# Performance work log

Measured on AMD Instinct MI355X. Metric: run time of the kernel, lower is better.

Reference implementation:

```python
import jax, jax.numpy as jnp
import numpy as np

BN_EPS = 1e-5


def setup_inputs() -> dict:
    key = jax.random.key(0)
    ks = jax.random.split(key, 12)
    B, C, L, P = 8, 128, 4096, 96
    d = C // 8
    return {
        "x": jax.random.normal(ks[0], (B, C, 1), jnp.float32),
        "Wt": jax.random.normal(ks[1], (C, C, L), jnp.float32) * 0.02,
        "bt": jax.random.normal(ks[2], (C,), jnp.float32) * 0.02,
        "gamma": jnp.ones((C,), jnp.float32),
        "beta": jnp.zeros((C,), jnp.float32),
        "Wq": jax.random.normal(ks[3], (d, C), jnp.float32) * 0.05,
        "bq": jax.random.normal(ks[4], (d,), jnp.float32) * 0.02,
        "Wk": jax.random.normal(ks[5], (d, C), jnp.float32) * 0.05,
        "bk": jax.random.normal(ks[6], (d,), jnp.float32) * 0.02,
        "Wv": jax.random.normal(ks[7], (C, C), jnp.float32) * 0.05,
        "bv": jax.random.normal(ks[8], (C,), jnp.float32) * 0.02,
        "W2": jax.random.normal(ks[9], (P, C), jnp.float32) * 0.05,
        "b2": jax.random.normal(ks[10], (P,), jnp.float32) * 0.02,
    }


def reference(x, Wt, bt, gamma, beta, Wq, bq, Wk, bk, Wv, bv, W2, b2):
    # l1: ConvTranspose1d(C, C, kernel=L, stride=1) on input of length 1
    # out[b, o, l] = sum_i x[b, i, 0] * Wt[i, o, l] + bt[o]
    h = jnp.einsum('bi,iol->bol', x[:, :, 0], Wt) + bt[None, :, None]  # [B,C,L]
    # BatchNorm1d (training mode: batch stats, biased variance)
    mean = jnp.mean(h, axis=(0, 2), keepdims=True)
    var = jnp.mean((h - mean) ** 2, axis=(0, 2), keepdims=True)
    h = (h - mean) * jax.lax.rsqrt(var + BN_EPS)
    h = h * gamma[None, :, None] + beta[None, :, None]
    h = jax.nn.relu(h)
    # Self_Attn: 1x1 conv projections
    q = jnp.einsum('qc,bcl->bql', Wq, h) + bq[None, :, None]   # [B,d,L]
    k = jnp.einsum('qc,bcl->bql', Wk, h) + bk[None, :, None]   # [B,d,L]
    v = jnp.einsum('oc,bcl->bol', Wv, h) + bv[None, :, None]   # [B,C,L]
    energy = jnp.einsum('bdl,bdm->blm', q, k)                  # [B,L,L]
    attn = jax.nn.softmax(energy, axis=-1)
    out = jnp.einsum('bcm,blm->bcl', v, attn)                  # [B,C,L]
    # l2: Conv1d(C -> P, kernel=1)
    y = jnp.einsum('pc,bcl->bpl', W2, out) + b2[None, :, None]  # [B,P,L]
    return y
```

## Files before the change

### kernel.cpp

```cpp
#include <hip/hip_runtime.h>

#define B_ 8
#define C_ 128
#define L_ 4096
#define P_ 96
#define D_ 16

typedef __attribute__((ext_vector_type(8))) short short8;
typedef __attribute__((ext_vector_type(16))) float float16v;

__device__ __forceinline__ unsigned short f2bf(float f) {
  unsigned int u = __float_as_uint(f);
  u += 0x7fff + ((u >> 16) & 1);
  return (unsigned short)(u >> 16);
}

constexpr size_t OFF_H      = 0;
constexpr size_t OFF_PSUM   = 16777216;
constexpr size_t OFF_PSUMSQ = OFF_PSUM + 8192;
constexpr size_t OFF_SCALE  = OFF_PSUMSQ + 8192;
constexpr size_t OFF_SHIFT  = OFF_SCALE + 512;
constexpr size_t OFF_WALLT  = OFF_SHIFT + 512;
constexpr size_t OFF_BALL   = OFF_WALLT + 65536;
constexpr size_t OFF_QT     = OFF_BALL + 512;
constexpr size_t OFF_KT     = OFF_QT + 1048576;
constexpr size_t OFF_V2     = OFF_KT + 1048576;

__global__ __launch_bounds__(128) void k_prep(
    const float* __restrict__ Wq, const float* __restrict__ bq,
    const float* __restrict__ Wk, const float* __restrict__ bk,
    const float* __restrict__ Wv, const float* __restrict__ bv,
    const float* __restrict__ W2,
    float* __restrict__ wallT, float* __restrict__ ball)
{
  const int r = blockIdx.x;
  const int c = threadIdx.x;
  float wv;
  if (r < 16) {
    wv = Wq[r * C_ + c];
  } else if (r < 32) {
    wv = Wk[(r - 16) * C_ + c];
  } else {
    const int p = r - 32;
    float s = 0.f;
    for (int o = 0; o < C_; ++o) s += W2[p * C_ + o] * Wv[o * C_ + c];
    wv = s;
  }
  wallT[c * C_ + r] = wv;
  if (c == 0) {
    float bb;
    if (r < 16)      bb = bq[r];
    else if (r < 32) bb = bk[r - 16];
    else {
      const int p = r - 32;
      float s = 0.f;
      for (int o = 0; o < C_; ++o) s += W2[p * C_ + o] * bv[o];
      bb = s;
    }
    ball[r] = bb;
  }
}

__global__ __launch_bounds__(256) void k_conv(
    const float* __restrict__ x, const float* __restrict__ Wt,
    float* __restrict__ h, float* __restrict__ psum, float* __restrict__ psumsq)
{
  __shared__ float4 xs4[256];
  __shared__ float rs1[4], rs2[4];
  const int tid = threadIdx.x;
  const int o = blockIdx.y;
  const int l = blockIdx.x * 1024 + tid * 4;

  xs4[tid] = ((const float4*)x)[tid];
  __syncthreads();

  float4 acc[8];
#pragma unroll
  for (int bb = 0; bb < 8; ++bb) acc[bb] = (float4){0.f, 0.f, 0.f, 0.f};

  const float* wp = Wt + (size_t)o * L_ + l;
  const size_t stride = (size_t)C_ * L_;
#pragma unroll 2
  for (int i4 = 0; i4 < 32; ++i4) {
    const float4 w0 = *(const float4*)(wp + (size_t)(i4 * 4 + 0) * stride);
    const float4 w1 = *(const float4*)(wp + (size_t)(i4 * 4 + 1) * stride);
    const float4 w2 = *(const float4*)(wp + (size_t)(i4 * 4 + 2) * stride);
    const float4 w3 = *(const float4*)(wp + (size_t)(i4 * 4 + 3) * stride);
#pragma unroll
    for (int bb = 0; bb < 8; ++bb) {
      const float4 xb = xs4[bb * 32 + i4];
      acc[bb].x += xb.x * w0.x + xb.y * w1.x + xb.z * w2.x + xb.w * w3.x;
      acc[bb].y += xb.x * w0.y + xb.y * w1.y + xb.z * w2.y + xb.w * w3.y;
      acc[bb].z += xb.x * w0.z + xb.y * w1.z + xb.z * w2.z + xb.w * w3.z;
      acc[bb].w += xb.x * w0.w + xb.y * w1.w + xb.z * w2.w + xb.w * w3.w;
    }
  }
  float s1 = 0.f, s2 = 0.f;
#pragma unroll
  for (int bb = 0; bb < 8; ++bb) {
    *(float4*)(h + ((size_t)(bb * C_ + o)) * L_ + l) = acc[bb];
    s1 += acc[bb].x + acc[bb].y + acc[bb].z + acc[bb].w;
    s2 += acc[bb].x * acc[bb].x + acc[bb].y * acc[bb].y
        + acc[bb].z * acc[bb].z + acc[bb].w * acc[bb].w;
  }
  for (int off = 1; off < 64; off <<= 1) {
    s1 += __shfl_xor(s1, off);
    s2 += __shfl_xor(s2, off);
  }
  if ((tid & 63) == 0) { rs1[tid >> 6] = s1; rs2[tid >> 6] = s2; }
  __syncthreads();
  if (tid == 0) {
    psum[o * 4 + blockIdx.x]   = rs1[0] + rs1[1] + rs1[2] + rs1[3];
    psumsq[o * 4 + blockIdx.x] = rs2[0] + rs2[1] + rs2[2] + rs2[3];
  }
}

__global__ __launch_bounds__(128) void k_bn(
    const float* __restrict__ psum, const float* __restrict__ psumsq,
    const float* __restrict__ gamma, const float* __restrict__ beta,
    float* __restrict__ scale, float* __restrict__ shift)
{
  const int c = threadIdx.x;
  float s1 = 0.f, s2 = 0.f;
  for (int t = 0; t < 4; ++t) { s1 += psum[c * 4 + t]; s2 += psumsq[c * 4 + t]; }
  const float inv = 1.f / 32768.f;
  const float mean = s1 * inv;
  const float var  = s2 * inv - mean * mean;
  const float sc   = rsqrtf(var + 1e-5f) * gamma[c];
  scale[c] = sc;
  shift[c] = beta[c] - mean * sc;
}

__global__ __launch_bounds__(256) void k_proj(
    const float* __restrict__ h, const float* __restrict__ scale,
    const float* __restrict__ shift, const float* __restrict__ wallT,
    const float* __restrict__ ball,
    unsigned short* __restrict__ qT, unsigned short* __restrict__ kT,
    unsigned short* __restrict__ v2w)
{
  const int b = blockIdx.y;
  const int l0 = blockIdx.x * 64;
  const int tid = threadIdx.x;
  const int wu = __builtin_amdgcn_readfirstlane(tid) >> 6;
  const int lane = tid & 63;
  const int l = l0 + lane;

  float acc[32];
#pragma unroll
  for (int r = 0; r < 32; ++r) acc[r] = ball[wu * 32 + r];

#pragma unroll 2
  for (int c = 0; c < C_; ++c) {
    const float hv = h[((size_t)(b * C_ + c)) * L_ + l];
    const float hn = fmaxf(hv * scale[c] + shift[c], 0.f);
    const float* wrow = wallT + c * C_ + wu * 32;
#pragma unroll
    for (int r = 0; r < 32; ++r) acc[r] += wrow[r] * hn;
  }

  if (wu == 0) {
    const size_t row = (size_t)(b * L_ + l) * D_;
    short8 v0, v1;
#pragma unroll
    for (int r = 0; r < 8; ++r) {
      v0[r] = (short)f2bf(acc[r] * 1.44269504f);
      v1[r] = (short)f2bf(acc[8 + r] * 1.44269504f);
    }
    *(short8*)(qT + row) = v0;  *(short8*)(qT + row + 8) = v1;
#pragma unroll
    for (int r = 0; r < 8; ++r) { v0[r] = (short)f2bf(acc[16 + r]); v1[r] = (short)f2bf(acc[24 + r]); }
    *(short8*)(kT + row) = v0;  *(short8*)(kT + row + 8) = v1;
  } else {
    const int pbase = wu * 32 - 32;
#pragma unroll
    for (int r = 0; r < 32; ++r)
      v2w[((size_t)(b * P_ + pbase + r)) * L_ + l] = f2bf(acc[r]);
  }
}

__global__ __launch_bounds__(1024, 4) void k_attn(
    const unsigned short* __restrict__ qT, const unsigned short* __restrict__ kT,
    const unsigned short* __restrict__ v2w, const float* __restrict__ b2,
    float* __restrict__ y)
{
  __shared__ float ldsO[P_ * 128];
  __shared__ float ldsL[128];

  const int b = blockIdx.y;
  const int l0 = blockIdx.x * 128;
  const int tid = threadIdx.x;
  const int w  = tid >> 6;
  const int qg = w & 3;
  const int ms = w >> 2;
  const int lane = tid & 63;
  const int col = lane & 31;
  const int hh  = lane >> 5;

#pragma unroll
  for (int i = 0; i < 12; ++i) ldsO[tid + i * 1024] = 0.f;
  if (tid < 128) ldsL[tid] = 0.f;
  __syncthreads();

  const int lq = l0 + qg * 32 + col;
  const short8 qf = *(const short8*)(qT + ((size_t)(b * L_ + lq)) * D_ + hh * 8);

  float16v oacc[3];
#pragma unroll
  for (int pt = 0; pt < 3; ++pt)
#pragma unroll
    for (int r = 0; r < 16; ++r) oacc[pt][r] = 0.f;
  float lsum = 0.f;

  const unsigned short* kbase =
      kT + ((size_t)(b * L_ + ms * 1024 + col)) * D_ + hh * 8;
  const unsigned short* vbb = v2w + (size_t)(b * P_ + col) * L_;

#pragma unroll 1
  for (int it = 0; it < 32; ++it) {
    const short8 kf = *(const short8*)(kbase + (size_t)it * 32 * D_);
    float16v zero;
#pragma unroll
    for (int r = 0; r < 16; ++r) zero[r] = 0.f;
    const float16v s = __builtin_amdgcn_mfma_f32_32x32x16_bf16(kf, qf, zero, 0, 0, 0);

    unsigned dw[8];
#pragma unroll
    for (int g = 0; g < 8; ++g) {
      const float e0 = __builtin_amdgcn_exp2f(s[2 * g]);
      const float e1 = __builtin_amdgcn_exp2f(s[2 * g + 1]);
      lsum += e0 + e1;
      const unsigned u0 = __float_as_uint(e0) + 0x8000u;
      const unsigned u1 = __float_as_uint(e1) + 0x8000u;
      dw[g] = __builtin_amdgcn_perm(u1, u0, 0x07060302u);
    }

    const int mbase = ms * 1024 + it * 32;
#pragma unroll
    for (int mt = 0; mt < 2; ++mt) {
      const unsigned t0 = hh ? dw[4 * mt + 0] : dw[4 * mt + 2];
      const unsigned t1 = hh ? dw[4 * mt + 1] : dw[4 * mt + 3];
      const unsigned r0 = (unsigned)__shfl_xor((int)t0, 32);
      const unsigned r1 = (unsigned)__shfl_xor((int)t1, 32);
      union { int4 i; short8 s8; } pu;
      pu.i.x = hh ? (int)r0 : (int)dw[4 * mt + 0];
      pu.i.y = hh ? (int)r1 : (int)dw[4 * mt + 1];
      pu.i.z = hh ? (int)dw[4 * mt + 2] : (int)r0;
      pu.i.w = hh ? (int)dw[4 * mt + 3] : (int)r1;
      const short8 pf = pu.s8;

      const size_t moff = (size_t)(mbase + mt * 16 + hh * 8);
#pragma unroll
      for (int pt = 0; pt < 3; ++pt) {
        const short8 vf = *(const short8*)(vbb + (size_t)pt * 32 * L_ + moff);
        oacc[pt] = __builtin_amdgcn_mfma_f32_32x32x16_bf16(vf, pf, oacc[pt], 0, 0, 0);
      }
    }
  }

  atomicAdd(&ldsL[qg * 32 + col], lsum);
#pragma unroll
  for (int pt = 0; pt < 3; ++pt)
#pragma unroll
    for (int r = 0; r < 16; ++r) {
      const int p = (r & 3) + 8 * (r >> 2) + 4 * hh + 32 * pt;
      atomicAdd(&ldsO[p * 128 + qg * 32 + col], oacc[pt][r]);
    }
  __syncthreads();

#pragma unroll
  for (int i = 0; i < 12; ++i) {
    const int idx = tid + i * 1024;
    const int p = idx >> 7;
    const int l = idx & 127;
    y[((size_t)(b * P_ + p)) * L_ + l0 + l] = ldsO[idx] / ldsL[l] + b2[p];
  }
}

extern "C" void kernel_launch(void* const* d_in, const int* in_sizes, int n_in,
                              void* d_out, int out_size, void* d_ws, size_t ws_size,
                              hipStream_t stream) {
  (void)in_sizes; (void)n_in; (void)out_size; (void)ws_size;
  const float* x     = (const float*)d_in[0];
  const float* Wt    = (const float*)d_in[1];
  const float* gamma = (const float*)d_in[3];
  const float* beta  = (const float*)d_in[4];
  const float* Wq    = (const float*)d_in[5];
  const float* bq    = (const float*)d_in[6];
  const float* Wk    = (const float*)d_in[7];
  const float* bk    = (const float*)d_in[8];
  const float* Wv    = (const float*)d_in[9];
  const float* bv    = (const float*)d_in[10];
  const float* W2    = (const float*)d_in[11];
  const float* b2    = (const float*)d_in[12];
  float* y = (float*)d_out;

  char* ws = (char*)d_ws;
  float* h       = (float*)(ws + OFF_H);
  float* psum    = (float*)(ws + OFF_PSUM);
  float* psumsq  = (float*)(ws + OFF_PSUMSQ);
  float* scale   = (float*)(ws + OFF_SCALE);
  float* shift   = (float*)(ws + OFF_SHIFT);
  float* wallT   = (float*)(ws + OFF_WALLT);
  float* ball    = (float*)(ws + OFF_BALL);
  unsigned short* qT  = (unsigned short*)(ws + OFF_QT);
  unsigned short* kT  = (unsigned short*)(ws + OFF_KT);
  unsigned short* v2w = (unsigned short*)(ws + OFF_V2);

  k_prep<<<128, 128, 0, stream>>>(Wq, bq, Wk, bk, Wv, bv, W2, wallT, ball);
  k_conv<<<dim3(4, 128), 256, 0, stream>>>(x, Wt, h, psum, psumsq);
  k_bn<<<1, 128, 0, stream>>>(psum, psumsq, gamma, beta, scale, shift);
  k_proj<<<dim3(64, 8), 256, 0, stream>>>(h, scale, shift, wallT, ball, qT, kT, v2w);
  k_attn<<<dim3(32, 8), 1024, 0, stream>>>(qT, kT, v2w, b2, y);
}
```

Baseline: 580.5 us.

## Prefetch and stage loads across conv, projection and attention kernels

The conv kernel now double-buffers the weight loads and staggers the starting input-channel index per block, so concurrent blocks hit different DRAM regions. The projection kernel stages the normalized activations in shared memory with vectorized loads and writes v2w through shared memory, giving coalesced 8-byte stores instead of scattered 2-byte ones. The attention loop prefetches the next K fragment, issues all V loads ahead of the score MFMA, and uses the hardware packed bf16 convert when it is available. The prep loops gain unroll pragmas. These changes raise register and LDS pressure, which may lower occupancy.

```diff
diff --git a/kernel.cpp b/kernel.cpp
--- a/kernel.cpp
+++ b/kernel.cpp
@@ -43,6 +43,7 @@
   } else {
     const int p = r - 32;
     float s = 0.f;
+#pragma unroll 8
     for (int o = 0; o < C_; ++o) s += W2[p * C_ + o] * Wv[o * C_ + c];
     wv = s;
   }
@@ -54,6 +55,7 @@
     else {
       const int p = r - 32;
       float s = 0.f;
+#pragma unroll 8
       for (int o = 0; o < C_; ++o) s += W2[p * C_ + o] * bv[o];
       bb = s;
     }
@@ -80,19 +82,29 @@
 
   const float* wp = Wt + (size_t)o * L_ + l;
   const size_t stride = (size_t)C_ * L_;
+  const int phase = (blockIdx.y + blockIdx.x * 8) & 31;
+
+  float4 wbuf[2][4];
+#pragma unroll
+  for (int q = 0; q < 4; ++q)
+    wbuf[0][q] = *(const float4*)(wp + (size_t)(phase * 4 + q) * stride);
+
 #pragma unroll 2
-  for (int i4 = 0; i4 < 32; ++i4) {
-    const float4 w0 = *(const float4*)(wp + (size_t)(i4 * 4 + 0) * stride);
-    const float4 w1 = *(const float4*)(wp + (size_t)(i4 * 4 + 1) * stride);
-    const float4 w2 = *(const float4*)(wp + (size_t)(i4 * 4 + 2) * stride);
-    const float4 w3 = *(const float4*)(wp + (size_t)(i4 * 4 + 3) * stride);
+  for (int g = 0; g < 32; ++g) {
+    const int cur = g & 1, nb = cur ^ 1;
+    const int in4 = ((phase + g + 1) & 31) * 4;
+#pragma unroll
+    for (int q = 0; q < 4; ++q)
+      wbuf[nb][q] = *(const float4*)(wp + (size_t)(in4 + q) * stride);
+
+    const int ic = (phase + g) & 31;
 #pragma unroll
     for (int bb = 0; bb < 8; ++bb) {
-      const float4 xb = xs4[bb * 32 + i4];
-      acc[bb].x += xb.x * w0.x + xb.y * w1.x + xb.z * w2.x + xb.w * w3.x;
-      acc[bb].y += xb.x * w0.y + xb.y * w1.y + xb.z * w2.y + xb.w * w3.y;
-      acc[bb].z += xb.x * w0.z + xb.y * w1.z + xb.z * w2.z + xb.w * w3.z;
-      acc[bb].w += xb.x * w0.w + xb.y * w1.w + xb.z * w2.w + xb.w * w3.w;
+      const float4 xb = xs4[bb * 32 + ic];
+      acc[bb].x += xb.x * wbuf[cur][0].x + xb.y * wbuf[cur][1].x + xb.z * wbuf[cur][2].x + xb.w * wbuf[cur][3].x;
+      acc[bb].y += xb.x * wbuf[cur][0].y + xb.y * wbuf[cur][1].y + xb.z * wbuf[cur][2].y + xb.w * wbuf[cur][3].y;
+      acc[bb].z += xb.x * wbuf[cur][0].z + xb.y * wbuf[cur][1].z + xb.z * wbuf[cur][2].z + xb.w * wbuf[cur][3].z;
+      acc[bb].w += xb.x * wbuf[cur][0].w + xb.y * wbuf[cur][1].w + xb.z * wbuf[cur][2].w + xb.w * wbuf[cur][3].w;
     }
   }
   float s1 = 0.f, s2 = 0.f;
@@ -138,9 +150,29 @@
     unsigned short* __restrict__ qT, unsigned short* __restrict__ kT,
     unsigned short* __restrict__ v2w)
 {
+  __shared__ __align__(16) char sm[128 * 68 * 4];
+  float* hn = (float*)sm;
+  unsigned short* v2s = (unsigned short*)sm;
+
   const int b = blockIdx.y;
   const int l0 = blockIdx.x * 64;
   const int tid = threadIdx.x;
+
+#pragma unroll
+  for (int i = 0; i < 8; ++i) {
+    const int idx = tid + i * 256;
+    const int c = idx >> 4, lq = (idx & 15) * 4;
+    const float4 hv = *(const float4*)(h + ((size_t)(b * C_ + c)) * L_ + l0 + lq);
+    const float sc = scale[c], sh = shift[c];
+    float4 r;
+    r.x = fmaxf(hv.x * sc + sh, 0.f);
+    r.y = fmaxf(hv.y * sc + sh, 0.f);
+    r.z = fmaxf(hv.z * sc + sh, 0.f);
+    r.w = fmaxf(hv.w * sc + sh, 0.f);
+    *(float4*)(hn + c * 68 + lq) = r;
+  }
+  __syncthreads();
+
   const int wu = __builtin_amdgcn_readfirstlane(tid) >> 6;
   const int lane = tid & 63;
   const int l = l0 + lane;
@@ -149,14 +181,14 @@
 #pragma unroll
   for (int r = 0; r < 32; ++r) acc[r] = ball[wu * 32 + r];
 
-#pragma unroll 2
+#pragma unroll 4
   for (int c = 0; c < C_; ++c) {
-    const float hv = h[((size_t)(b * C_ + c)) * L_ + l];
-    const float hn = fmaxf(hv * scale[c] + shift[c], 0.f);
+    const float hv = hn[c * 68 + lane];
     const float* wrow = wallT + c * C_ + wu * 32;
 #pragma unroll
-    for (int r = 0; r < 32; ++r) acc[r] += wrow[r] * hn;
-  }
+    for (int r = 0; r < 32; ++r) acc[r] += wrow[r] * hv;
+  }
+  __syncthreads();
 
   if (wu == 0) {
     const size_t row = (size_t)(b * L_ + l) * D_;
@@ -174,7 +206,16 @@
     const int pbase = wu * 32 - 32;
 #pragma unroll
     for (int r = 0; r < 32; ++r)
-      v2w[((size_t)(b * P_ + pbase + r)) * L_ + l] = f2bf(acc[r]);
+      v2s[(pbase + r) * 72 + lane] = f2bf(acc[r]);
+  }
+  __syncthreads();
+
+#pragma unroll
+  for (int i = 0; i < 6; ++i) {
+    const int idx = tid + i * 256;
+    const int p = idx >> 4, off = (idx & 15) * 4;
+    const uint2 val = *(const uint2*)(v2s + p * 72 + off);
+    *(uint2*)(v2w + ((size_t)(b * P_ + p)) * L_ + l0 + off) = val;
   }
 }
 
@@ -215,13 +256,26 @@
       kT + ((size_t)(b * L_ + ms * 1024 + col)) * D_ + hh * 8;
   const unsigned short* vbb = v2w + (size_t)(b * P_ + col) * L_;
 
-#pragma unroll 1
+  short8 kf_cur = *(const short8*)(kbase);
+
+#pragma unroll 2
   for (int it = 0; it < 32; ++it) {
-    const short8 kf = *(const short8*)(kbase + (size_t)it * 32 * D_);
+    const int itn = (it + 1) & 31;
+    const short8 kf_nxt = *(const short8*)(kbase + (size_t)itn * 32 * D_);
+
+    const int mbase = ms * 1024 + it * 32;
+    short8 vf[6];
+#pragma unroll
+    for (int mt = 0; mt < 2; ++mt)
+#pragma unroll
+      for (int pt = 0; pt < 3; ++pt)
+        vf[mt * 3 + pt] = *(const short8*)(vbb + (size_t)pt * 32 * L_
+                                           + (size_t)(mbase + mt * 16 + hh * 8));
+
     float16v zero;
 #pragma unroll
     for (int r = 0; r < 16; ++r) zero[r] = 0.f;
-    const float16v s = __builtin_amdgcn_mfma_f32_32x32x16_bf16(kf, qf, zero, 0, 0, 0);
+    const float16v s = __builtin_amdgcn_mfma_f32_32x32x16_bf16(kf_cur, qf, zero, 0, 0, 0);
 
     unsigned dw[8];
 #pragma unroll
@@ -229,12 +283,17 @@
       const float e0 = __builtin_amdgcn_exp2f(s[2 * g]);
       const float e1 = __builtin_amdgcn_exp2f(s[2 * g + 1]);
       lsum += e0 + e1;
+#if __has_builtin(__builtin_amdgcn_cvt_pk_bf16_f32)
+      typedef __attribute__((ext_vector_type(2))) __bf16 bf162;
+      const bf162 pk = __builtin_amdgcn_cvt_pk_bf16_f32(e0, e1);
+      dw[g] = *(const unsigned*)&pk;
+#else
       const unsigned u0 = __float_as_uint(e0) + 0x8000u;
       const unsigned u1 = __float_as_uint(e1) + 0x8000u;
       dw[g] = __builtin_amdgcn_perm(u1, u0, 0x07060302u);
-    }
-
-    const int mbase = ms * 1024 + it * 32;
+#endif
+    }
+
 #pragma unroll
     for (int mt = 0; mt < 2; ++mt) {
       const unsigned t0 = hh ? dw[4 * mt + 0] : dw[4 * mt + 2];
@@ -247,14 +306,11 @@
       pu.i.z = hh ? (int)dw[4 * mt + 2] : (int)r0;
       pu.i.w = hh ? (int)dw[4 * mt + 3] : (int)r1;
       const short8 pf = pu.s8;
-
-      const size_t moff = (size_t)(mbase + mt * 16 + hh * 8);
-#pragma unroll
-      for (int pt = 0; pt < 3; ++pt) {
-        const short8 vf = *(const short8*)(vbb + (size_t)pt * 32 * L_ + moff);
-        oacc[pt] = __builtin_amdgcn_mfma_f32_32x32x16_bf16(vf, pf, oacc[pt], 0, 0, 0);
-      }
-    }
+#pragma unroll
+      for (int pt = 0; pt < 3; ++pt)
+        oacc[pt] = __builtin_amdgcn_mfma_f32_32x32x16_bf16(vf[mt * 3 + pt], pf, oacc[pt], 0, 0, 0);
+    }
+    kf_cur = kf_nxt;
   }
 
   atomicAdd(&ldsL[qg * 32 + col], lsum);
```

Measured after the change: 577.9 us. No clear change (-0.4%).
